# Kernel optimization log

Hardware: AMD Instinct MI355X
Metric: run time of the kernel (lower is better)

The kernel has to match this reference:

```python
import jax, jax.numpy as jnp
import numpy as np

N_NODES = 100000
N_EDGES = 2500000
IN_CH = 32
HID = 16
OUT_CH = 32


def setup_inputs() -> dict:
    key = jax.random.key(0)
    ks = jax.random.split(key, 10)
    x = jax.random.normal(ks[0], (N_NODES, IN_CH), dtype=jnp.float32)
    edge_index = jax.random.randint(ks[1], (2, N_EDGES), 0, N_NODES, dtype=jnp.int64)
    # conv1 MLP: Linear(in,16) -> ReLU -> Linear(16,out)
    W1 = jax.random.normal(ks[2], (IN_CH, HID), dtype=jnp.float32) / np.sqrt(IN_CH)
    b1 = jnp.zeros((HID,), dtype=jnp.float32)
    W2 = jax.random.normal(ks[3], (HID, OUT_CH), dtype=jnp.float32) / np.sqrt(HID)
    b2 = jnp.zeros((OUT_CH,), dtype=jnp.float32)
    # conv2 MLP: Linear(out,16) -> ReLU -> Linear(16,out)
    W3 = jax.random.normal(ks[4], (OUT_CH, HID), dtype=jnp.float32) / np.sqrt(OUT_CH)
    b3 = jnp.zeros((HID,), dtype=jnp.float32)
    W4 = jax.random.normal(ks[5], (HID, OUT_CH), dtype=jnp.float32) / np.sqrt(HID)
    b4 = jnp.zeros((OUT_CH,), dtype=jnp.float32)
    return {"x": x, "edge_index": edge_index, "W1": W1, "b1": b1, "W2": W2,
            "b2": b2, "W3": W3, "b3": b3, "W4": W4, "b4": b4}


def _gin_conv(x, src, dst, W_a, b_a, W_b, b_b):
    # GINConv (eps=0): nn((1+eps)*x + sum_{j in N(i)} x_j)
    agg = jax.ops.segment_sum(x[src], dst, num_segments=x.shape[0])  # [N, d]
    h = x + agg
    h = jnp.maximum(h @ W_a + b_a, 0.0)  # Linear -> ReLU
    return h @ W_b + b_b                 # Linear


def reference(x, edge_index, W1, b1, W2, b2, W3, b3, W4, b4):
    src, dst = edge_index[0], edge_index[1]
    h = _gin_conv(x, src, dst, W1, b1, W2, b2)
    h = jnp.maximum(h, 0.0)  # F.relu between convs
    out = _gin_conv(h, src, dst, W3, b3, W4, b4)
    return out
```

## Files before the change

kernel.cpp:

```cpp
#include <hip/hip_runtime.h>

typedef unsigned short ushort_t;
typedef unsigned int uint_t;

#define BKT_SHIFT 7
#define BKT_NODES 128
#define NBKT_MAX 800
#define BCAP 4096
#define EPB 8192

__device__ __forceinline__ ushort_t f2bf(float f) {
    unsigned u = __float_as_uint(f);
    unsigned r = (u + 0x7FFFu + ((u >> 16) & 1u)) >> 16;
    return (ushort_t)r;
}
__device__ __forceinline__ float bflo(uint_t u) { return __uint_as_float(u << 16); }
__device__ __forceinline__ float bfhi(uint_t u) { return __uint_as_float(u & 0xFFFF0000u); }

__global__ __launch_bounds__(512) void scatter_lin(
    const int* __restrict__ src, const int* __restrict__ dst,
    int* __restrict__ gcnt, int* __restrict__ staged,
    const float4* __restrict__ x4, const float* __restrict__ W,
    ushort_t* __restrict__ z, int E, int SBLK, int N, int NBKT)
{
    __shared__ float sW[512];
    __shared__ int lcnt[NBKT_MAX];
    __shared__ int lbase[NBKT_MAX];
    __shared__ int lcur[NBKT_MAX];
    __shared__ int bpre[NBKT_MAX];
    __shared__ int swsum[512];
    __shared__ int sstage[EPB];
    int t = threadIdx.x, blk = blockIdx.x;
    if (blk < SBLK) {
        for (int b = t; b < NBKT; b += 512) { lcnt[b] = 0; lcur[b] = 0; }
        __syncthreads();
        int e0 = blk * EPB;
        int rd[16], rs[16];
        #pragma unroll
        for (int i = 0; i < 16; ++i) {
            int e = e0 + i * 512 + t;
            bool ok = (e < E);
            rd[i] = ok ? dst[e] : -1;
            rs[i] = ok ? src[e] : 0;
            if (ok) atomicAdd(&lcnt[rd[i] >> BKT_SHIFT], 1);
        }
        __syncthreads();
        for (int b = t; b < NBKT; b += 512)
            lbase[b] = atomicAdd(&gcnt[b], lcnt[b]);
        int j0 = t * 2;
        int c0 = (j0     < NBKT) ? lcnt[j0]     : 0;
        int c1 = (j0 + 1 < NBKT) ? lcnt[j0 + 1] : 0;
        swsum[t] = c0 + c1;
        __syncthreads();
        for (int off = 1; off < 512; off <<= 1) {
            int add = (t >= off) ? swsum[t - off] : 0;
            __syncthreads();
            swsum[t] += add;
            __syncthreads();
        }
        int excl = swsum[t] - (c0 + c1);
        if (j0     < NBKT) bpre[j0]     = excl;
        if (j0 + 1 < NBKT) bpre[j0 + 1] = excl + c0;
        __syncthreads();
        #pragma unroll
        for (int i = 0; i < 16; ++i) {
            if (rd[i] >= 0) {
                int b = rd[i] >> BKT_SHIFT;
                int r = atomicAdd(&lcur[b], 1);
                sstage[bpre[b] + r] = ((rd[i] & (BKT_NODES - 1)) << 24) | rs[i];
            }
        }
        __syncthreads();
        int wid = t >> 6, lane = t & 63;
        for (int b = wid; b < NBKT; b += 8) {
            int cnt = lcnt[b];
            int gb  = lbase[b];
            int lb  = bpre[b];
            for (int k = lane; k < cnt; k += 64) {
                int gs = gb + k;
                if (gs < BCAP)
                    staged[(size_t)b * BCAP + gs] = sstage[lb + k];
            }
        }
    } else {
        sW[t] = W[t];
        __syncthreads();
        int n = (blk - SBLK) * 512 + t;
        if (n >= N) return;
        float a[16];
        #pragma unroll
        for (int c = 0; c < 16; ++c) a[c] = 0.f;
        const float4* xr = x4 + (size_t)n * 8;
        #pragma unroll
        for (int k4 = 0; k4 < 8; ++k4) {
            float4 xv = xr[k4];
            #pragma unroll
            for (int c = 0; c < 16; ++c) {
                a[c] += xv.x * sW[(k4 * 4 + 0) * 16 + c];
                a[c] += xv.y * sW[(k4 * 4 + 1) * 16 + c];
                a[c] += xv.z * sW[(k4 * 4 + 2) * 16 + c];
                a[c] += xv.w * sW[(k4 * 4 + 3) * 16 + c];
            }
        }
        uint_t w[8];
        #pragma unroll
        for (int i2 = 0; i2 < 8; ++i2)
            w[i2] = (uint_t)f2bf(a[2 * i2]) | ((uint_t)f2bf(a[2 * i2 + 1]) << 16);
        uint4* zo = (uint4*)(z + (size_t)n * 16);
        uint4 q0; q0.x = w[0]; q0.y = w[1]; q0.z = w[2]; q0.w = w[3];
        uint4 q1; q1.x = w[4]; q1.y = w[5]; q1.z = w[6]; q1.w = w[7];
        zo[0] = q0;
        zo[1] = q1;
    }
}


__device__ __forceinline__ void gather_acc(
    const uint4* __restrict__ zp, const int* __restrict__ scol,
    int k, int ke, int sl, float* acc)
{
    for (; k + 8 <= ke; k += 8) {
        uint4 uu[8];
        #pragma unroll
        for (int j = 0; j < 8; ++j)
            uu[j] = zp[(size_t)scol[k + j] * 2 + sl];
        #pragma unroll
        for (int j = 0; j < 8; ++j) {
            acc[0] += bflo(uu[j].x); acc[1] += bfhi(uu[j].x);
            acc[2] += bflo(uu[j].y); acc[3] += bfhi(uu[j].y);
            acc[4] += bflo(uu[j].z); acc[5] += bfhi(uu[j].z);
            acc[6] += bflo(uu[j].w); acc[7] += bfhi(uu[j].w);
        }
    }
    for (; k < ke; ++k) {
        uint4 u = zp[(size_t)scol[k] * 2 + sl];
        acc[0] += bflo(u.x); acc[1] += bfhi(u.x);
        acc[2] += bflo(u.y); acc[3] += bfhi(u.y);
        acc[4] += bflo(u.z); acc[5] += bfhi(u.z);
        acc[6] += bflo(u.w); acc[7] += bfhi(u.w);
    }
}

__device__ __forceinline__ void mlp_front(
    const float* acc, const float* sba, const float* sWb, const float* sbb,
    int sl, float* o)
{
    float h[8], hp[8];
    #pragma unroll
    for (int j = 0; j < 8; ++j) h[j] = fmaxf(acc[j] + sba[sl * 8 + j], 0.f);
    #pragma unroll
    for (int j = 0; j < 8; ++j) hp[j] = __shfl_xor(h[j], 1);
    float hl[8], hh[8];
    #pragma unroll
    for (int j = 0; j < 8; ++j) {
        hl[j] = sl ? hp[j] : h[j];
        hh[j] = sl ? h[j] : hp[j];
    }
    int ocb = sl * 16;
    #pragma unroll
    for (int i = 0; i < 16; ++i) o[i] = sbb[ocb + i];
    #pragma unroll
    for (int j = 0; j < 8; ++j) {
        #pragma unroll
        for (int i = 0; i < 16; ++i) {
            o[i] += hl[j] * sWb[j * 32 + ocb + i];
            o[i] += hh[j] * sWb[(j + 8) * 32 + ocb + i];
        }
    }
}

__global__ __launch_bounds__(256) void agg1(
    const ushort_t* __restrict__ zin, const int* __restrict__ staged,
    const int* __restrict__ gcnt,
    int* __restrict__ colg, int2* __restrict__ rp2,
    const float* __restrict__ ba,
    const float* __restrict__ Wb, const float* __restrict__ bb,
    const float* __restrict__ Wc,
    ushort_t* __restrict__ z2, int N)
{
    __shared__ float sWb[512];
    __shared__ float sWc[512];
    __shared__ float sba[16], sbb[32];
    __shared__ int scnt[512], srel[512], scur[512];
    __shared__ int sns[128];
    __shared__ int snode[129];
    __shared__ int scol[BCAP];

    int t = threadIdx.x;
    sWb[t] = Wb[t];  sWb[t + 256] = Wb[t + 256];
    sWc[t] = Wc[t];  sWc[t + 256] = Wc[t + 256];
    if (t < 16) sba[t] = ba[t];
    if (t < 32) sbb[t] = bb[t];
    scnt[t] = 0; scnt[t + 256] = 0;
    scur[t] = 0; scur[t + 256] = 0;
    __syncthreads();

    int b = blockIdx.x;
    int m = min(gcnt[b], BCAP);
    const int* sp = staged + (size_t)b * BCAP;

    for (int i = t; i < m; i += 256) {
        int v = sp[i];
        atomicAdd(&scnt[(((unsigned)v >> 24) << 2) | (v & 3)], 1);
    }
    __syncthreads();
    int c0 = 0, c1 = 0, c2 = 0, c3 = 0, tot = 0;
    if (t < 128) {
        c0 = scnt[t * 4 + 0]; c1 = scnt[t * 4 + 1];
        c2 = scnt[t * 4 + 2]; c3 = scnt[t * 4 + 3];
        tot = c0 + c1 + c2 + c3;
        sns[t] = tot;
    }
    __syncthreads();
    for (int off = 1; off < 128; off <<= 1) {
        int add = (t < 128 && t >= off) ? sns[t - off] : 0;
        __syncthreads();
        if (t < 128) sns[t] += add;
        __syncthreads();
    }
    if (t < 128) {
        int excl = sns[t] - tot;
        srel[t * 4 + 0] = excl;
        srel[t * 4 + 1] = excl + c0;
        srel[t * 4 + 2] = excl + c0 + c1;
        srel[t * 4 + 3] = excl + c0 + c1 + c2;
        snode[t] = excl;
        if (t == 127) snode[128] = sns[127];
    }
    __syncthreads();
    for (int i = t; i < m; i += 256) {
        int v = sp[i];
        int idx = (((unsigned)v >> 24) << 2) | (v & 3);
        int p = srel[idx] + atomicAdd(&scur[idx], 1);
        scol[p] = v & 0xFFFFFF;
    }
    __syncthreads();
    for (int i = t; i < m; i += 256)
        colg[(size_t)b * BCAP + i] = scol[i];
    int base = b << BKT_SHIFT;
    if (t < 128 && base + t < N)
        rp2[base + t] = make_int2(b * BCAP + snode[t], b * BCAP + snode[t + 1]);

    int ln = t >> 1, sl = t & 1;
    int n = base + ln;
    if (n < N) {
        const uint4* zp = (const uint4*)zin;
        uint4 us = zp[(size_t)n * 2 + sl];
        float acc[8] = { bflo(us.x), bfhi(us.x), bflo(us.y), bfhi(us.y),
                         bflo(us.z), bfhi(us.z), bflo(us.w), bfhi(us.w) };
        gather_acc(zp, scol, snode[ln], snode[ln + 1], sl, acc);
        float o[16];
        mlp_front(acc, sba, sWb, sbb, sl, o);
        float p[16];
        #pragma unroll
        for (int zc = 0; zc < 16; ++zc) p[zc] = 0.f;
        int ocb = sl * 16;
        #pragma unroll
        for (int i = 0; i < 16; ++i) {
            float r = fmaxf(o[i], 0.f);
            #pragma unroll
            for (int zc = 0; zc < 16; ++zc)
                p[zc] += r * sWc[(ocb + i) * 16 + zc];
        }
        float pm[8], po[8];
        #pragma unroll
        for (int k = 0; k < 8; ++k) {
            pm[k] = sl ? p[8 + k] : p[k];
            po[k] = sl ? p[k] : p[8 + k];
        }
        #pragma unroll
        for (int k = 0; k < 8; ++k) po[k] = __shfl_xor(po[k], 1);
        uint_t w[4];
        #pragma unroll
        for (int k = 0; k < 4; ++k) {
            float zA = pm[2 * k]     + po[2 * k];
            float zB = pm[2 * k + 1] + po[2 * k + 1];
            w[k] = (uint_t)f2bf(zA) | ((uint_t)f2bf(zB) << 16);
        }
        uint4 q; q.x = w[0]; q.y = w[1]; q.z = w[2]; q.w = w[3];
        ((uint4*)z2)[(size_t)n * 2 + sl] = q;
    }
}

__global__ __launch_bounds__(256) void agg2(
    const ushort_t* __restrict__ zin, const int* __restrict__ colg,
    const int2* __restrict__ rp2,
    const float* __restrict__ ba,
    const float* __restrict__ Wb, const float* __restrict__ bb,
    float* __restrict__ out, int N)
{
    __shared__ float sWb[512];
    __shared__ float sba[16], sbb[32];
    __shared__ int scol[BCAP];

    int t = threadIdx.x;
    sWb[t] = Wb[t];  sWb[t + 256] = Wb[t + 256];
    if (t < 16) sba[t] = ba[t];
    if (t < 32) sbb[t] = bb[t];

    int b = blockIdx.x;
    int base = b << BKT_SHIFT;
    int kb = b * BCAP;
    int last = min(base + BKT_NODES, N) - 1;
    int m = rp2[last].y - kb;
    for (int i = t; i < m; i += 256)
        scol[i] = __builtin_nontemporal_load(colg + (size_t)kb + i);
    __syncthreads();

    int ln = t >> 1, sl = t & 1;
    int n = base + ln;
    if (n < N) {
        const uint4* zp = (const uint4*)zin;
        uint4 us = zp[(size_t)n * 2 + sl];
        float acc[8] = { bflo(us.x), bfhi(us.x), bflo(us.y), bfhi(us.y),
                         bflo(us.z), bfhi(us.z), bflo(us.w), bfhi(us.w) };
        int2 r = rp2[n];
        gather_acc(zp, scol, r.x - kb, r.y - kb, sl, acc);
        float o[16];
        mlp_front(acc, sba, sWb, sbb, sl, o);
        float* op = out + (size_t)n * 32 + sl * 16;
        #pragma unroll
        for (int i = 0; i < 16; ++i)
            __builtin_nontemporal_store(o[i], op + i);
    }
}


extern "C" void kernel_launch(void* const* d_in, const int* in_sizes, int n_in,
                              void* d_out, int out_size, void* d_ws, size_t ws_size,
                              hipStream_t stream) {
    const float* x  = (const float*)d_in[0];
    const int*   ei = (const int*)d_in[1];
    const float* W1 = (const float*)d_in[2];
    const float* b1 = (const float*)d_in[3];
    const float* W2 = (const float*)d_in[4];
    const float* b2 = (const float*)d_in[5];
    const float* W3 = (const float*)d_in[6];
    const float* b3 = (const float*)d_in[7];
    const float* W4 = (const float*)d_in[8];
    const float* b4 = (const float*)d_in[9];

    const int N = in_sizes[0] / 32;
    const int E = in_sizes[1] / 2;
    const int* src = ei;
    const int* dst = ei + E;

    const int NBKT = (N + BKT_NODES - 1) >> BKT_SHIFT;
    const int SBLK = (E + EPB - 1) / EPB;
    const int LINB = (N + 511) / 512;

    char* ws = (char*)d_ws;
    size_t o = 0;
    auto alloc = [&](size_t bytes) -> char* {
        o = (o + 255) & ~(size_t)255;
        char* r = ws + o;
        o += bytes;
        return r;
    };
    int*      gcnt   = (int*)     alloc(4 * (size_t)NBKT);
    int*      staged = (int*)     alloc(4 * (size_t)NBKT * BCAP);
    int*      colg   = (int*)     alloc(4 * (size_t)NBKT * BCAP);
    int2*     rp2    = (int2*)    alloc(8 * (size_t)N);
    ushort_t* zb     = (ushort_t*)alloc(2 * (size_t)N * 16);
    ushort_t* z2b    = (ushort_t*)alloc(2 * (size_t)N * 16);

    hipMemsetAsync(gcnt, 0, 4 * (size_t)NBKT, stream);

    scatter_lin<<<SBLK + LINB, 512, 0, stream>>>(
        src, dst, gcnt, staged, (const float4*)x, W1, zb, E, SBLK, N, NBKT);

    agg1<<<NBKT, 256, 0, stream>>>(
        zb, staged, gcnt, colg, rp2, b1, W2, b2, W3, z2b, N);
    agg2<<<NBKT, 256, 0, stream>>>(
        z2b, colg, rp2, b3, W4, b4, (float*)d_out, N);
}
```

Baseline: 183.7 us.

## Scatter edges directly to global buckets and re-sort per layer instead of storing CSR

The edge-binning kernel drops the LDS staging buffer and block-wide prefix scan and writes each edge straight to its global bucket slot, using a shared-memory atomic offset. Both aggregation layers now run one templated kernel that re-reads the staged buckets and re-sorts them in shared memory. This removes the writes and reads of the colg/rp2 CSR arrays. The trade-offs are uncoalesced global writes in the scatter and a repeated per-bucket counting sort in the second layer.

```diff
diff --git a/kernel.cpp b/kernel.cpp
--- a/kernel.cpp
+++ b/kernel.cpp
@@ -27,9 +27,6 @@
     __shared__ int lcnt[NBKT_MAX];
     __shared__ int lbase[NBKT_MAX];
     __shared__ int lcur[NBKT_MAX];
-    __shared__ int bpre[NBKT_MAX];
-    __shared__ int swsum[512];
-    __shared__ int sstage[EPB];
     int t = threadIdx.x, blk = blockIdx.x;
     if (blk < SBLK) {
         for (int b = t; b < NBKT; b += 512) { lcnt[b] = 0; lcur[b] = 0; }
@@ -47,39 +44,15 @@
         __syncthreads();
         for (int b = t; b < NBKT; b += 512)
             lbase[b] = atomicAdd(&gcnt[b], lcnt[b]);
-        int j0 = t * 2;
-        int c0 = (j0     < NBKT) ? lcnt[j0]     : 0;
-        int c1 = (j0 + 1 < NBKT) ? lcnt[j0 + 1] : 0;
-        swsum[t] = c0 + c1;
-        __syncthreads();
-        for (int off = 1; off < 512; off <<= 1) {
-            int add = (t >= off) ? swsum[t - off] : 0;
-            __syncthreads();
-            swsum[t] += add;
-            __syncthreads();
-        }
-        int excl = swsum[t] - (c0 + c1);
-        if (j0     < NBKT) bpre[j0]     = excl;
-        if (j0 + 1 < NBKT) bpre[j0 + 1] = excl + c0;
         __syncthreads();
         #pragma unroll
         for (int i = 0; i < 16; ++i) {
             if (rd[i] >= 0) {
                 int b = rd[i] >> BKT_SHIFT;
-                int r = atomicAdd(&lcur[b], 1);
-                sstage[bpre[b] + r] = ((rd[i] & (BKT_NODES - 1)) << 24) | rs[i];
-            }
-        }
-        __syncthreads();
-        int wid = t >> 6, lane = t & 63;
-        for (int b = wid; b < NBKT; b += 8) {
-            int cnt = lcnt[b];
-            int gb  = lbase[b];
-            int lb  = bpre[b];
-            for (int k = lane; k < cnt; k += 64) {
-                int gs = gb + k;
-                if (gs < BCAP)
-                    staged[(size_t)b * BCAP + gs] = sstage[lb + k];
+                int r = lbase[b] + atomicAdd(&lcur[b], 1);
+                if (r < BCAP)
+                    staged[(size_t)b * BCAP + r] =
+                        ((rd[i] & (BKT_NODES - 1)) << 24) | rs[i];
             }
         }
     } else {
@@ -169,14 +142,15 @@
     }
 }
 
-__global__ __launch_bounds__(256) void agg1(
+
+template <bool CHAIN>
+__global__ __launch_bounds__(256) void agg_sort_mlp(
     const ushort_t* __restrict__ zin, const int* __restrict__ staged,
     const int* __restrict__ gcnt,
-    int* __restrict__ colg, int2* __restrict__ rp2,
     const float* __restrict__ ba,
     const float* __restrict__ Wb, const float* __restrict__ bb,
     const float* __restrict__ Wc,
-    ushort_t* __restrict__ z2, int N)
+    void* __restrict__ outv, int N)
 {
     __shared__ float sWb[512];
     __shared__ float sWc[512];
@@ -188,7 +162,7 @@
 
     int t = threadIdx.x;
     sWb[t] = Wb[t];  sWb[t + 256] = Wb[t + 256];
-    sWc[t] = Wc[t];  sWc[t + 256] = Wc[t + 256];
+    if (CHAIN) { sWc[t] = Wc[t];  sWc[t + 256] = Wc[t + 256]; }
     if (t < 16) sba[t] = ba[t];
     if (t < 32) sbb[t] = bb[t];
     scnt[t] = 0; scnt[t + 256] = 0;
@@ -235,13 +209,9 @@
         scol[p] = v & 0xFFFFFF;
     }
     __syncthreads();
-    for (int i = t; i < m; i += 256)
-        colg[(size_t)b * BCAP + i] = scol[i];
+
+    int ln = t >> 1, sl = t & 1;
     int base = b << BKT_SHIFT;
-    if (t < 128 && base + t < N)
-        rp2[base + t] = make_int2(b * BCAP + snode[t], b * BCAP + snode[t + 1]);
-
-    int ln = t >> 1, sl = t & 1;
     int n = base + ln;
     if (n < N) {
         const uint4* zp = (const uint4*)zin;
@@ -251,77 +221,41 @@
         gather_acc(zp, scol, snode[ln], snode[ln + 1], sl, acc);
         float o[16];
         mlp_front(acc, sba, sWb, sbb, sl, o);
-        float p[16];
-        #pragma unroll
-        for (int zc = 0; zc < 16; ++zc) p[zc] = 0.f;
-        int ocb = sl * 16;
-        #pragma unroll
-        for (int i = 0; i < 16; ++i) {
-            float r = fmaxf(o[i], 0.f);
-            #pragma unroll
-            for (int zc = 0; zc < 16; ++zc)
-                p[zc] += r * sWc[(ocb + i) * 16 + zc];
-        }
-        float pm[8], po[8];
-        #pragma unroll
-        for (int k = 0; k < 8; ++k) {
-            pm[k] = sl ? p[8 + k] : p[k];
-            po[k] = sl ? p[k] : p[8 + k];
-        }
-        #pragma unroll
-        for (int k = 0; k < 8; ++k) po[k] = __shfl_xor(po[k], 1);
-        uint_t w[4];
-        #pragma unroll
-        for (int k = 0; k < 4; ++k) {
-            float zA = pm[2 * k]     + po[2 * k];
-            float zB = pm[2 * k + 1] + po[2 * k + 1];
-            w[k] = (uint_t)f2bf(zA) | ((uint_t)f2bf(zB) << 16);
-        }
-        uint4 q; q.x = w[0]; q.y = w[1]; q.z = w[2]; q.w = w[3];
-        ((uint4*)z2)[(size_t)n * 2 + sl] = q;
-    }
-}
-
-__global__ __launch_bounds__(256) void agg2(
-    const ushort_t* __restrict__ zin, const int* __restrict__ colg,
-    const int2* __restrict__ rp2,
-    const float* __restrict__ ba,
-    const float* __restrict__ Wb, const float* __restrict__ bb,
-    float* __restrict__ out, int N)
-{
-    __shared__ float sWb[512];
-    __shared__ float sba[16], sbb[32];
-    __shared__ int scol[BCAP];
-
-    int t = threadIdx.x;
-    sWb[t] = Wb[t];  sWb[t + 256] = Wb[t + 256];
-    if (t < 16) sba[t] = ba[t];
-    if (t < 32) sbb[t] = bb[t];
-
-    int b = blockIdx.x;
-    int base = b << BKT_SHIFT;
-    int kb = b * BCAP;
-    int last = min(base + BKT_NODES, N) - 1;
-    int m = rp2[last].y - kb;
-    for (int i = t; i < m; i += 256)
-        scol[i] = __builtin_nontemporal_load(colg + (size_t)kb + i);
-    __syncthreads();
-
-    int ln = t >> 1, sl = t & 1;
-    int n = base + ln;
-    if (n < N) {
-        const uint4* zp = (const uint4*)zin;
-        uint4 us = zp[(size_t)n * 2 + sl];
-        float acc[8] = { bflo(us.x), bfhi(us.x), bflo(us.y), bfhi(us.y),
-                         bflo(us.z), bfhi(us.z), bflo(us.w), bfhi(us.w) };
-        int2 r = rp2[n];
-        gather_acc(zp, scol, r.x - kb, r.y - kb, sl, acc);
-        float o[16];
-        mlp_front(acc, sba, sWb, sbb, sl, o);
-        float* op = out + (size_t)n * 32 + sl * 16;
-        #pragma unroll
-        for (int i = 0; i < 16; ++i)
-            __builtin_nontemporal_store(o[i], op + i);
+        if (CHAIN) {
+            float p[16];
+            #pragma unroll
+            for (int zc = 0; zc < 16; ++zc) p[zc] = 0.f;
+            int ocb = sl * 16;
+            #pragma unroll
+            for (int i = 0; i < 16; ++i) {
+                float r = fmaxf(o[i], 0.f);
+                #pragma unroll
+                for (int zc = 0; zc < 16; ++zc)
+                    p[zc] += r * sWc[(ocb + i) * 16 + zc];
+            }
+            float pm[8], po[8];
+            #pragma unroll
+            for (int k = 0; k < 8; ++k) {
+                pm[k] = sl ? p[8 + k] : p[k];
+                po[k] = sl ? p[k] : p[8 + k];
+            }
+            #pragma unroll
+            for (int k = 0; k < 8; ++k) po[k] = __shfl_xor(po[k], 1);
+            uint_t w[4];
+            #pragma unroll
+            for (int k = 0; k < 4; ++k) {
+                float zA = pm[2 * k]     + po[2 * k];
+                float zB = pm[2 * k + 1] + po[2 * k + 1];
+                w[k] = (uint_t)f2bf(zA) | ((uint_t)f2bf(zB) << 16);
+            }
+            uint4 q; q.x = w[0]; q.y = w[1]; q.z = w[2]; q.w = w[3];
+            ((uint4*)outv)[(size_t)n * 2 + sl] = q;
+        } else {
+            float* op = (float*)outv + (size_t)n * 32 + sl * 16;
+            #pragma unroll
+            for (int i = 0; i < 16; ++i)
+                __builtin_nontemporal_store(o[i], op + i);
+        }
     }
 }
 
@@ -359,8 +293,6 @@
     };
     int*      gcnt   = (int*)     alloc(4 * (size_t)NBKT);
     int*      staged = (int*)     alloc(4 * (size_t)NBKT * BCAP);
-    int*      colg   = (int*)     alloc(4 * (size_t)NBKT * BCAP);
-    int2*     rp2    = (int2*)    alloc(8 * (size_t)N);
     ushort_t* zb     = (ushort_t*)alloc(2 * (size_t)N * 16);
     ushort_t* z2b    = (ushort_t*)alloc(2 * (size_t)N * 16);
 
@@ -369,8 +301,8 @@
     scatter_lin<<<SBLK + LINB, 512, 0, stream>>>(
         src, dst, gcnt, staged, (const float4*)x, W1, zb, E, SBLK, N, NBKT);
 
-    agg1<<<NBKT, 256, 0, stream>>>(
-        zb, staged, gcnt, colg, rp2, b1, W2, b2, W3, z2b, N);
-    agg2<<<NBKT, 256, 0, stream>>>(
-        z2b, colg, rp2, b3, W4, b4, (float*)d_out, N);
-}
+    agg_sort_mlp<true ><<<NBKT, 256, 0, stream>>>(
+        zb, staged, gcnt, b1, W2, b2, W3, z2b, N);
+    agg_sort_mlp<false><<<NBKT, 256, 0, stream>>>(
+        z2b, staged, gcnt, b3, W4, b4, nullptr, (float*)d_out, N);
+}
```

After: 180.0 us. 1.02x faster.
